# Optimization experiments

Measured on AMD Instinct MI355X. Metric: run time of the kernel, lower is better.

Reference implementation:

```python
import jax, jax.numpy as jnp
import numpy as np

B, L, C = 1, 4096, 1024
H = 16
D = C // H  # head_dim = 64


def setup_inputs() -> dict:
    key = jax.random.key(0)
    k1, k2, k3 = jax.random.split(key, 3)
    scale_in = 1.0 / np.sqrt(C)
    return {
        "x": jax.random.normal(k1, (B, L, C), dtype=jnp.float32),
        "Wqkv": jax.random.normal(k2, (C, 3 * C), dtype=jnp.float32) * scale_in,
        "bqkv": jnp.zeros((3 * C,), dtype=jnp.float32),
        "Wout": jax.random.normal(k3, (C, C), dtype=jnp.float32) * scale_in,
        "bout": jnp.zeros((C,), dtype=jnp.float32),
    }


def reference(x, Wqkv, bqkv, Wout, bout):
    Bx, Lx, Cx = x.shape
    qkv = x @ Wqkv + bqkv                             # [B, L, 3C]
    qkv = qkv.reshape(Bx, Lx, 3, H, D)
    qkv = jnp.transpose(qkv, (2, 0, 3, 1, 4))         # [3, B, H, L, D]
    q, k, v = qkv[0], qkv[1], qkv[2]
    scores = jnp.einsum("bhqd,bhkd->bhqk", q, k) / jnp.sqrt(jnp.float32(D))
    # causal mask: strictly upper triangle -> -inf
    causal = jnp.triu(jnp.ones((Lx, Lx), dtype=bool), k=1)
    scores = jnp.where(causal, -jnp.inf, scores)
    attn = jax.nn.softmax(scores, axis=-1)            # [B, H, L, L]
    out = jnp.einsum("bhqk,bhkd->bhqd", attn, v)      # [B, H, L, D]
    out = jnp.transpose(out, (0, 2, 1, 3)).reshape(Bx, Lx, Cx)
    return out @ Wout + bout
```

## Files before the change

kernel.cpp:

```cpp
#include <hip/hip_runtime.h>
#include <hip/hip_bf16.h>

typedef unsigned short u16;
typedef __bf16 bf16x8 __attribute__((ext_vector_type(8)));
typedef float f32x4 __attribute__((ext_vector_type(4)));

#define L_SEQ 4096
#define CDIM  1024
#define NH    16
#define HD    64
#define N_QKV 3072
#define ATT_STRIDE 72
#define TILE_HW (64 * ATT_STRIDE)

static __device__ __forceinline__ float bf2f(u16 u) {
    union { float f; unsigned int i; } v; v.i = ((unsigned int)u) << 16; return v.f;
}
static __device__ __forceinline__ u16 f2bf(float f) {
    union { float f; unsigned int i; } v; v.f = f;
    unsigned int u = v.i;
    return (u16)((u + 0x7fffu + ((u >> 16) & 1u)) >> 16);
}
static __device__ __forceinline__ float exp2_(float x) {
    return __builtin_exp2f(x);
}

static __device__ __forceinline__ f32x4 mfma16x16x32(bf16x8 a, bf16x8 b, f32x4 c) {
    return __builtin_amdgcn_mfma_f32_16x16x32_bf16(a, b, c, 0, 0, 0);
}

typedef const __attribute__((address_space(1))) unsigned int* gas_u32;
typedef __attribute__((address_space(3))) unsigned int* las_u32;
static __device__ __forceinline__ void gload_lds16(const u16* g, u16* l) {
    __builtin_amdgcn_global_load_lds((gas_u32)g, (las_u32)l, 16, 0, 0);
}

__global__ __launch_bounds__(256) void k_cast_x(const float* __restrict__ src,
                                                u16* __restrict__ dst, int n8) {
    int i = blockIdx.x * 256 + threadIdx.x;
    if (i >= n8) return;
    const float4* s = (const float4*)(src + (size_t)i * 8);
    float4 a = s[0], b = s[1];
    u16 o[8] = { f2bf(a.x), f2bf(a.y), f2bf(a.z), f2bf(a.w),
                 f2bf(b.x), f2bf(b.y), f2bf(b.z), f2bf(b.w) };
    *(uint4*)(dst + (size_t)i * 8) = *(uint4*)o;
}

__global__ __launch_bounds__(256) void k_transpose_cast(const float* __restrict__ src,
                                                        u16* __restrict__ dst,
                                                        int R, int C) {
    __shared__ u16 tile[32][33];
    int c0 = blockIdx.x * 32, r0 = blockIdx.y * 32;
    int tx = threadIdx.x & 31, ty = threadIdx.x >> 5;
#pragma unroll
    for (int i = 0; i < 32; i += 8)
        tile[ty + i][tx] = f2bf(src[(size_t)(r0 + ty + i) * C + c0 + tx]);
    __syncthreads();
#pragma unroll
    for (int i = 0; i < 32; i += 8)
        dst[(size_t)(c0 + ty + i) * R + r0 + tx] = tile[tx][ty + i];
}

__global__ __launch_bounds__(256) void k_transpose_v(const u16* __restrict__ qkv,
                                                     u16* __restrict__ vt) {
    __shared__ u16 tile[32][33];
    int k0 = blockIdx.x * 32, d0 = blockIdx.y * 32, h = blockIdx.z;
    int tx = threadIdx.x & 31, ty = threadIdx.x >> 5;
#pragma unroll
    for (int i = 0; i < 32; i += 8)
        tile[ty + i][tx] = qkv[(size_t)(k0 + ty + i) * N_QKV + 2 * CDIM + h * HD + d0 + tx];
    __syncthreads();
#pragma unroll
    for (int i = 0; i < 32; i += 8)
        vt[(size_t)(h * HD + d0 + ty + i) * L_SEQ + k0 + tx] = tile[tx][ty + i];
}

template <typename OutT>
__global__ __launch_bounds__(256) void k_gemm_bt(const u16* __restrict__ A,
                                                 const u16* __restrict__ Bt,
                                                 const float* __restrict__ bias,
                                                 OutT* __restrict__ Cmat,
                                                 int M, int N, int K) {
    __shared__ alignas(16) u16 As[2][128 * 32];
    __shared__ alignas(16) u16 Bs[2][128 * 32];
    int t = threadIdx.x;
    int n0 = blockIdx.x * 128, m0 = blockIdx.y * 128;
    int l = t & 63, w = t >> 6;
    int wm = (w >> 1) * 64, wn = (w & 1) * 64;
    int lr = l & 15, lq = l >> 4;

    const f32x4 vzero = {0.f, 0.f, 0.f, 0.f};
    f32x4 acc[4][4];
#pragma unroll
    for (int mi = 0; mi < 4; mi++)
#pragma unroll
        for (int ni = 0; ni < 4; ni++) acc[mi][ni] = vzero;

    int ar = t >> 2;
    int ac = (t & 3) * 8;
    const u16* Ag = A + (size_t)(m0 + ar) * K + ac;
    const u16* Bg = Bt + (size_t)(n0 + ar) * K + ac;

    int nk = K >> 5;

    auto stage = [&](int kt, int bu) {
        int k0 = kt << 5;
        gload_lds16(Ag + k0,                  &As[bu][t * 8]);
        gload_lds16(Ag + (size_t)64 * K + k0, &As[bu][t * 8 + 64 * 32]);
        gload_lds16(Bg + k0,                  &Bs[bu][t * 8]);
        gload_lds16(Bg + (size_t)64 * K + k0, &Bs[bu][t * 8 + 64 * 32]);
    };

    stage(0, 0);
    __syncthreads();

    int bu = 0;
    for (int kt = 0; kt < nk; ++kt) {
        if (kt + 1 < nk) stage(kt + 1, bu ^ 1);

        bf16x8 af[4], bfr[4];
#pragma unroll
        for (int mi = 0; mi < 4; mi++)
            af[mi] = *(const bf16x8*)&As[bu][(wm + mi * 16 + lr) * 32 + lq * 8];
#pragma unroll
        for (int ni = 0; ni < 4; ni++)
            bfr[ni] = *(const bf16x8*)&Bs[bu][(wn + ni * 16 + lr) * 32 + lq * 8];
#pragma unroll
        for (int mi = 0; mi < 4; mi++)
#pragma unroll
            for (int ni = 0; ni < 4; ni++)
                acc[mi][ni] = mfma16x16x32(af[mi], bfr[ni], acc[mi][ni]);

        __syncthreads();
        bu ^= 1;
    }

#pragma unroll
    for (int ni = 0; ni < 4; ni++) {
        int col = n0 + wn + ni * 16 + lr;
        float bv = bias[col];
#pragma unroll
        for (int mi = 0; mi < 4; mi++) {
            int row = m0 + wm + mi * 16 + lq * 4;
#pragma unroll
            for (int r = 0; r < 4; r++) {
                float v = acc[mi][ni][r] + bv;
                if constexpr (sizeof(OutT) == 2)
                    Cmat[(size_t)(row + r) * N + col] = f2bf(v);
                else
                    Cmat[(size_t)(row + r) * N + col] = v;
            }
        }
    }
}

__global__ __launch_bounds__(512, 4) void k_attn(const u16* __restrict__ qkv,
                                                 const u16* __restrict__ vt,
                                                 u16* __restrict__ attn) {
    __shared__ alignas(16) u16 Ks[2][2 * TILE_HW];
    __shared__ alignas(16) u16 Vs[2][2 * TILE_HW];

    int t = threadIdx.x;
    int l = t & 63, w = t >> 6;
    int g = w >> 2;
    int ww = w & 3;
    int h = blockIdx.x;
    int pair = blockIdx.y;
    int lr = l & 15, lq = l >> 4;
    int tg = t & 255;
    int row8 = tg >> 3;
    int ch = (tg & 7) * 8;
    int qloc = ww * 16 + lr;

    const f32x4 vzero = {0.f, 0.f, 0.f, 0.f};
    const u16* Kbase = qkv + (size_t)row8 * N_QKV + CDIM + h * HD + ch;
    const u16* Vbase = vt + (size_t)(h * HD + row8) * L_SEQ + ch;
    u16* KsG = Ks[g];
    u16* VsG = Vs[g];

#pragma unroll
    for (int phase = 0; phase < 2; phase++) {
        int tile = phase ? (63 - pair) : pair;
        int q0 = tile * 64;
        int nkv = tile + 1;
        int h0 = (nkv + 1) >> 1;
        int myBeg = g ? h0 : 0;
        int myCnt = g ? (nkv - h0) : h0;

        const float SC = 0.125f * 1.44269504089f;
        bf16x8 bq[2];
        {
            const u16* Qg = qkv + (size_t)(q0 + qloc) * N_QKV + h * HD + lq * 8;
            union { uint4 u; u16 hh[8]; } q0u, q1u;
            q0u.u = *(const uint4*)(Qg);
            q1u.u = *(const uint4*)(Qg + 32);
            union { bf16x8 v; __bf16 e[8]; } f0, f1;
#pragma unroll
            for (int j = 0; j < 8; j++) {
                f0.e[j] = (__bf16)(bf2f(q0u.hh[j]) * SC);
                f1.e[j] = (__bf16)(bf2f(q1u.hh[j]) * SC);
            }
            bq[0] = f0.v; bq[1] = f1.v;
        }

        f32x4 o[4];
#pragma unroll
        for (int dt = 0; dt < 4; dt++) o[dt] = vzero;
        float m_i = -1e30f, l_i = 0.f;

        uint4 rk0 = {0,0,0,0}, rk1 = {0,0,0,0}, rv0 = {0,0,0,0}, rv1 = {0,0,0,0};
        if (myCnt > 0) {
            const u16* Kg = Kbase + (size_t)(myBeg * 64) * N_QKV;
            rk0 = *(const uint4*)Kg;
            rk1 = *(const uint4*)(Kg + (size_t)32 * N_QKV);
            const u16* Vg = Vbase + myBeg * 64;
            rv0 = *(const uint4*)Vg;
            rv1 = *(const uint4*)(Vg + (size_t)32 * L_SEQ);
            *(uint4*)&KsG[row8 * ATT_STRIDE + ch]        = rk0;
            *(uint4*)&KsG[(row8 + 32) * ATT_STRIDE + ch] = rk1;
            *(uint4*)&VsG[row8 * ATT_STRIDE + ch]        = rv0;
            *(uint4*)&VsG[(row8 + 32) * ATT_STRIDE + ch] = rv1;
            if (myCnt > 1) {
                int k1 = (myBeg + 1) * 64;
                Kg = Kbase + (size_t)k1 * N_QKV;
                rk0 = *(const uint4*)Kg;
                rk1 = *(const uint4*)(Kg + (size_t)32 * N_QKV);
                Vg = Vbase + k1;
                rv0 = *(const uint4*)Vg;
                rv1 = *(const uint4*)(Vg + (size_t)32 * L_SEQ);
            }
        }
        __syncthreads();

        for (int j = 0; j < h0; ++j) {
            int cur = (j & 1) ? TILE_HW : 0;
            if (j + 1 < myCnt) {
                int nxt = TILE_HW - cur;
                *(uint4*)&KsG[nxt + row8 * ATT_STRIDE + ch]        = rk0;
                *(uint4*)&KsG[nxt + (row8 + 32) * ATT_STRIDE + ch] = rk1;
                *(uint4*)&VsG[nxt + row8 * ATT_STRIDE + ch]        = rv0;
                *(uint4*)&VsG[nxt + (row8 + 32) * ATT_STRIDE + ch] = rv1;
            }
            if (j + 2 < myCnt) {
                int k1 = (myBeg + j + 2) * 64;
                const u16* Kg = Kbase + (size_t)k1 * N_QKV;
                rk0 = *(const uint4*)Kg;
                rk1 = *(const uint4*)(Kg + (size_t)32 * N_QKV);
                const u16* Vg = Vbase + k1;
                rv0 = *(const uint4*)Vg;
                rv1 = *(const uint4*)(Vg + (size_t)32 * L_SEQ);
            }

            if (j < myCnt) {
                const u16* Kc = KsG + cur;
                const u16* Vc = VsG + cur;

                f32x4 s[4];
#pragma unroll
                for (int nt = 0; nt < 4; nt++) s[nt] = vzero;
                __builtin_amdgcn_s_setprio(1);
#pragma unroll
                for (int ks = 0; ks < 2; ks++)
#pragma unroll
                    for (int nt = 0; nt < 4; nt++) {
                        bf16x8 ak = *(const bf16x8*)&Kc[(nt * 16 + lr) * ATT_STRIDE + ks * 32 + lq * 8];
                        s[nt] = mfma16x16x32(ak, bq[ks], s[nt]);
                    }
                __builtin_amdgcn_s_setprio(0);

                bool diag = (((myBeg + j) * 64) == q0);
                float tmax = -1e30f;
                if (diag) {
#pragma unroll
                    for (int nt = 0; nt < 4; nt++)
#pragma unroll
                        for (int r = 0; r < 4; r++) {
                            float v = s[nt][r];
                            if (nt * 16 + lq * 4 + r > qloc) v = -1e30f;
                            s[nt][r] = v;
                            tmax = fmaxf(tmax, v);
                        }
                } else {
#pragma unroll
                    for (int nt = 0; nt < 4; nt++)
#pragma unroll
                        for (int r = 0; r < 4; r++) tmax = fmaxf(tmax, s[nt][r]);
                }

                if (!__all(tmax <= m_i + 11.0f)) {
                    float tq = fmaxf(tmax, __shfl_xor(tmax, 16));
                    tq = fmaxf(tq, __shfl_xor(tq, 32));
                    float mnew = fmaxf(m_i, tq);
                    float alpha = exp2_(m_i - mnew);
                    l_i *= alpha;
#pragma unroll
                    for (int dt = 0; dt < 4; dt++)
#pragma unroll
                        for (int r = 0; r < 4; r++) o[dt][r] *= alpha;
                    m_i = mnew;
                }

#pragma unroll
                for (int nt = 0; nt < 4; nt++)
#pragma unroll
                    for (int r = 0; r < 4; r++) {
                        float e = exp2_(s[nt][r] - m_i);
                        s[nt][r] = e;
                        l_i += e;
                    }

                __builtin_amdgcn_s_setprio(1);
#pragma unroll
                for (int a = 0; a < 2; a++) {
                    union { bf16x8 v; __bf16 e[8]; } bp;
#pragma unroll
                    for (int r = 0; r < 4; r++) {
                        bp.e[r]     = (__bf16)s[2 * a][r];
                        bp.e[r + 4] = (__bf16)s[2 * a + 1][r];
                    }
#pragma unroll
                    for (int dt = 0; dt < 4; dt++) {
                        union { bf16x8 v; uint2 u2[2]; } av;
                        const u16* vrow = &Vc[(dt * 16 + lr) * ATT_STRIDE + a * 32 + lq * 4];
                        av.u2[0] = *(const uint2*)(vrow);
                        av.u2[1] = *(const uint2*)(vrow + 16);
                        o[dt] = mfma16x16x32(av.v, bp.v, o[dt]);
                    }
                }
                __builtin_amdgcn_s_setprio(0);
            }
            __syncthreads();
        }

        l_i += __shfl_xor(l_i, 16);
        l_i += __shfl_xor(l_i, 32);

        float* mb1 = (float*)Ks[1];
        float* mb2 = (float*)Vs[1];
        if (g == 1) {
            float* p = mb1 + tg * 10;
            p[0] = m_i; p[1] = l_i;
#pragma unroll
            for (int r = 0; r < 4; r++) { p[2 + r] = o[0][r]; p[6 + r] = o[1][r]; }
            float* p2 = mb2 + tg * 8;
#pragma unroll
            for (int r = 0; r < 4; r++) { p2[r] = o[2][r]; p2[4 + r] = o[3][r]; }
        }
        __syncthreads();
        if (g == 0) {
            float* p = mb1 + tg * 10;
            float m1v = p[0], l1v = p[1];
            float mnew = fmaxf(m_i, m1v);
            float a0 = exp2_(m_i - mnew);
            float a1 = exp2_(m1v - mnew);
            float lm = l_i * a0 + l1v * a1;
            float* p2 = mb2 + tg * 8;
            f32x4 o1[4];
#pragma unroll
            for (int r = 0; r < 4; r++) {
                o1[0][r] = p[2 + r]; o1[1][r] = p[6 + r];
                o1[2][r] = p2[r];    o1[3][r] = p2[4 + r];
            }
            float inv = 1.0f / lm;
            int qg = q0 + qloc;
#pragma unroll
            for (int dt = 0; dt < 4; dt++) {
                union { u16 hh[4]; uint2 u2; __bf16 e[4]; } eo;
#pragma unroll
                for (int r = 0; r < 4; r++)
                    eo.e[r] = (__bf16)((o[dt][r] * a0 + o1[dt][r] * a1) * inv);
                *(uint2*)&attn[(size_t)qg * CDIM + h * HD + dt * 16 + lq * 4] = eo.u2;
            }
        }
        __syncthreads();
    }
}

extern "C" void kernel_launch(void* const* d_in, const int* in_sizes, int n_in,
                              void* d_out, int out_size, void* d_ws, size_t ws_size,
                              hipStream_t stream) {
    const float* x    = (const float*)d_in[0];
    const float* Wqkv = (const float*)d_in[1];
    const float* bqkv = (const float*)d_in[2];
    const float* Wout = (const float*)d_in[3];
    const float* bout = (const float*)d_in[4];
    float* out = (float*)d_out;

    char* ws = (char*)d_ws;
    u16* qkv   = (u16*)(ws);
    u16* xb    = (u16*)(ws + 25165824);
    u16* attn  = xb;
    u16* vt    = (u16*)(ws + 33554432);
    u16* wqkvt = (u16*)(ws + 41943040);
    u16* woutt = (u16*)(ws + 48234496);

    k_cast_x<<<dim3(2048), 256, 0, stream>>>(x, xb, 524288);
    k_transpose_cast<<<dim3(96, 32), 256, 0, stream>>>(Wqkv, wqkvt, 1024, 3072);
    k_transpose_cast<<<dim3(32, 32), 256, 0, stream>>>(Wout, woutt, 1024, 1024);
    k_gemm_bt<u16><<<dim3(24, 32), 256, 0, stream>>>(xb, wqkvt, bqkv, qkv, 4096, 3072, 1024);
    k_transpose_v<<<dim3(128, 2, 16), 256, 0, stream>>>(qkv, vt);
    k_attn<<<dim3(16, 32), 512, 0, stream>>>(qkv, vt, attn);
    k_gemm_bt<float><<<dim3(8, 32), 256, 0, stream>>>(attn, woutt, bout, out, 4096, 1024, 1024);
}
```

Baseline: 225.3 us.

## Fuse V transpose into QKV GEMM epilogue and narrow output GEMM tile

The QKV projection GEMM now writes the V columns directly in transposed [d][L] layout from its epilogue, which removes the separate V transpose kernel and its extra read and write of V. The output projection GEMM uses a 128x64 tile instead of 128x128, doubling its grid to 512 blocks so more of the GPU is occupied. The costs are more A-tile reloads in the output GEMM and strided 8-byte stores for the fused V write.

New measurement: 228.2 us. About the same (+1.3%).

```diff
diff --git a/kernel.cpp b/kernel.cpp
--- a/kernel.cpp
+++ b/kernel.cpp
@@ -61,40 +61,28 @@
         dst[(size_t)(c0 + ty + i) * R + r0 + tx] = tile[tx][ty + i];
 }
 
-__global__ __launch_bounds__(256) void k_transpose_v(const u16* __restrict__ qkv,
-                                                     u16* __restrict__ vt) {
-    __shared__ u16 tile[32][33];
-    int k0 = blockIdx.x * 32, d0 = blockIdx.y * 32, h = blockIdx.z;
-    int tx = threadIdx.x & 31, ty = threadIdx.x >> 5;
-#pragma unroll
-    for (int i = 0; i < 32; i += 8)
-        tile[ty + i][tx] = qkv[(size_t)(k0 + ty + i) * N_QKV + 2 * CDIM + h * HD + d0 + tx];
-    __syncthreads();
-#pragma unroll
-    for (int i = 0; i < 32; i += 8)
-        vt[(size_t)(h * HD + d0 + ty + i) * L_SEQ + k0 + tx] = tile[tx][ty + i];
-}
-
-template <typename OutT>
+template <typename OutT, int BN, bool FUSE_VT>
 __global__ __launch_bounds__(256) void k_gemm_bt(const u16* __restrict__ A,
                                                  const u16* __restrict__ Bt,
                                                  const float* __restrict__ bias,
                                                  OutT* __restrict__ Cmat,
+                                                 u16* __restrict__ vt,
                                                  int M, int N, int K) {
+    constexpr int NI = BN / 32;
     __shared__ alignas(16) u16 As[2][128 * 32];
-    __shared__ alignas(16) u16 Bs[2][128 * 32];
+    __shared__ alignas(16) u16 Bs[2][BN * 32];
     int t = threadIdx.x;
-    int n0 = blockIdx.x * 128, m0 = blockIdx.y * 128;
+    int n0 = blockIdx.x * BN, m0 = blockIdx.y * 128;
     int l = t & 63, w = t >> 6;
-    int wm = (w >> 1) * 64, wn = (w & 1) * 64;
+    int wm = (w >> 1) * 64, wn = (w & 1) * (BN / 2);
     int lr = l & 15, lq = l >> 4;
 
     const f32x4 vzero = {0.f, 0.f, 0.f, 0.f};
-    f32x4 acc[4][4];
+    f32x4 acc[4][NI];
 #pragma unroll
     for (int mi = 0; mi < 4; mi++)
 #pragma unroll
-        for (int ni = 0; ni < 4; ni++) acc[mi][ni] = vzero;
+        for (int ni = 0; ni < NI; ni++) acc[mi][ni] = vzero;
 
     int ar = t >> 2;
     int ac = (t & 3) * 8;
@@ -108,7 +96,8 @@
         gload_lds16(Ag + k0,                  &As[bu][t * 8]);
         gload_lds16(Ag + (size_t)64 * K + k0, &As[bu][t * 8 + 64 * 32]);
         gload_lds16(Bg + k0,                  &Bs[bu][t * 8]);
-        gload_lds16(Bg + (size_t)64 * K + k0, &Bs[bu][t * 8 + 64 * 32]);
+        if constexpr (BN == 128)
+            gload_lds16(Bg + (size_t)64 * K + k0, &Bs[bu][t * 8 + 64 * 32]);
     };
 
     stage(0, 0);
@@ -118,37 +107,55 @@
     for (int kt = 0; kt < nk; ++kt) {
         if (kt + 1 < nk) stage(kt + 1, bu ^ 1);
 
-        bf16x8 af[4], bfr[4];
+        bf16x8 af[4], bfr[NI];
 #pragma unroll
         for (int mi = 0; mi < 4; mi++)
             af[mi] = *(const bf16x8*)&As[bu][(wm + mi * 16 + lr) * 32 + lq * 8];
 #pragma unroll
-        for (int ni = 0; ni < 4; ni++)
+        for (int ni = 0; ni < NI; ni++)
             bfr[ni] = *(const bf16x8*)&Bs[bu][(wn + ni * 16 + lr) * 32 + lq * 8];
 #pragma unroll
         for (int mi = 0; mi < 4; mi++)
 #pragma unroll
-            for (int ni = 0; ni < 4; ni++)
+            for (int ni = 0; ni < NI; ni++)
                 acc[mi][ni] = mfma16x16x32(af[mi], bfr[ni], acc[mi][ni]);
 
         __syncthreads();
         bu ^= 1;
     }
 
-#pragma unroll
-    for (int ni = 0; ni < 4; ni++) {
-        int col = n0 + wn + ni * 16 + lr;
-        float bv = bias[col];
-#pragma unroll
-        for (int mi = 0; mi < 4; mi++) {
-            int row = m0 + wm + mi * 16 + lq * 4;
-#pragma unroll
-            for (int r = 0; r < 4; r++) {
-                float v = acc[mi][ni][r] + bv;
-                if constexpr (sizeof(OutT) == 2)
-                    Cmat[(size_t)(row + r) * N + col] = f2bf(v);
-                else
-                    Cmat[(size_t)(row + r) * N + col] = v;
+    bool vpath = FUSE_VT && (n0 >= 2 * CDIM);
+    if (vpath) {
+#pragma unroll
+        for (int ni = 0; ni < NI; ni++) {
+            int col = n0 + wn + ni * 16 + lr;
+            float bv = bias[col];
+            int d = col - 2 * CDIM;
+#pragma unroll
+            for (int mi = 0; mi < 4; mi++) {
+                int row = m0 + wm + mi * 16 + lq * 4;
+                union { u16 hh[4]; uint2 u2; } eo;
+#pragma unroll
+                for (int r = 0; r < 4; r++) eo.hh[r] = f2bf(acc[mi][ni][r] + bv);
+                *(uint2*)&vt[(size_t)d * L_SEQ + row] = eo.u2;
+            }
+        }
+    } else {
+#pragma unroll
+        for (int ni = 0; ni < NI; ni++) {
+            int col = n0 + wn + ni * 16 + lr;
+            float bv = bias[col];
+#pragma unroll
+            for (int mi = 0; mi < 4; mi++) {
+                int row = m0 + wm + mi * 16 + lq * 4;
+#pragma unroll
+                for (int r = 0; r < 4; r++) {
+                    float v = acc[mi][ni][r] + bv;
+                    if constexpr (sizeof(OutT) == 2)
+                        Cmat[(size_t)(row + r) * N + col] = f2bf(v);
+                    else
+                        Cmat[(size_t)(row + r) * N + col] = v;
+                }
             }
         }
     }
@@ -397,8 +404,9 @@
     k_cast_x<<<dim3(2048), 256, 0, stream>>>(x, xb, 524288);
     k_transpose_cast<<<dim3(96, 32), 256, 0, stream>>>(Wqkv, wqkvt, 1024, 3072);
     k_transpose_cast<<<dim3(32, 32), 256, 0, stream>>>(Wout, woutt, 1024, 1024);
-    k_gemm_bt<u16><<<dim3(24, 32), 256, 0, stream>>>(xb, wqkvt, bqkv, qkv, 4096, 3072, 1024);
-    k_transpose_v<<<dim3(128, 2, 16), 256, 0, stream>>>(qkv, vt);
+    k_gemm_bt<u16, 128, true><<<dim3(24, 32), 256, 0, stream>>>(
+        xb, wqkvt, bqkv, qkv, vt, 4096, 3072, 1024);
     k_attn<<<dim3(16, 32), 512, 0, stream>>>(qkv, vt, attn);
-    k_gemm_bt<float><<<dim3(8, 32), 256, 0, stream>>>(attn, woutt, bout, out, 4096, 1024, 1024);
-}
+    k_gemm_bt<float, 64, false><<<dim3(16, 32), 256, 0, stream>>>(
+        attn, woutt, bout, out, nullptr, 4096, 1024, 1024);
+}
```
